# Kernel tuning notes

Measured on AMD Instinct MI355X. Metric: run time of the kernel, lower is better.

The kernel has to match this reference:

```python
import jax, jax.numpy as jnp
import numpy as np

OUT_F = 4096
IN_F = 4096
NNZ_PER_ROW = 205            # ortho_ratio 0.05 * IN_F
NNZ = OUT_F * NNZ_PER_ROW    # 839680
ALPHA = 1.0                  # self.alpha (privacy on)


def setup_inputs() -> dict:
    key = jax.random.key(0)
    k1, k2, k3, k4 = jax.random.split(key, 4)
    x = jax.random.normal(k1, (4, 2048, IN_F), dtype=jnp.float32)
    # offset-uint8 quantized weight (stored here as int32 in [0,256))
    base_packed = jax.random.randint(k2, (OUT_F, IN_F), 0, 256, dtype=jnp.int32)
    # per-output-row dequant scales (robust_max/127 -> small positive values)
    scales = jax.random.uniform(k3, (OUT_F,), dtype=jnp.float32, minval=1e-4, maxval=4e-3)
    # CSR sparse residual: uniform row occupancy, sorted col indices per row
    ortho_vals = (jax.random.normal(k4, (NNZ,), dtype=jnp.float32) * 0.01).astype(jnp.float16)
    rng = np.random.default_rng(0)
    cols = np.sort(rng.integers(0, IN_F, size=(OUT_F, NNZ_PER_ROW)), axis=1)
    ortho_indices = jnp.asarray(cols.reshape(-1).astype(np.int32))
    ortho_ptr = jnp.asarray((np.arange(OUT_F + 1) * NNZ_PER_ROW).astype(np.int32))
    return {
        "x": x,
        "base_packed": base_packed,
        "scales": scales,
        "ortho_vals": ortho_vals,
        "ortho_indices": ortho_indices,
        "ortho_ptr": ortho_ptr,
    }


def reference(x, base_packed, scales, ortho_vals, ortho_indices, ortho_ptr):
    orig_shape = x.shape
    x_flat = x.reshape(-1, IN_F).astype(jnp.float32)          # [T, IN_F]
    # dequantize int8 base weight: (u8 - 128) * scale_row
    w_base = (base_packed.astype(jnp.float32) - 128.0) * scales[:, None]  # [OUT_F, IN_F]
    # expand CSR row pointers -> per-nnz row ids (fixed total length, jit-safe)
    counts = jnp.diff(ortho_ptr)
    rows = jnp.repeat(jnp.arange(OUT_F, dtype=jnp.int32), counts,
                      total_repeat_length=ortho_vals.shape[0])
    # scatter sparse residual into dense weight (matches torch CSR->dense fallback)
    w_ortho = jnp.zeros((OUT_F, IN_F), jnp.float32).at[rows, ortho_indices].add(
        ortho_vals.astype(jnp.float32))
    w = w_base + ALPHA * w_ortho
    out = x_flat @ w.T                                         # [T, OUT_F]
    return out.reshape(orig_shape[:-1] + (OUT_F,)).astype(x.dtype)
```

## Files before the change

### kernel.cpp

```cpp
#include <hip/hip_runtime.h>
#include <hip/hip_fp16.h>

#define IN_F 4096
#define OUT_F 4096
#define TOK 8192
#define NNZ_PER_ROW 205
#define NNZ (OUT_F * NNZ_PER_ROW)

typedef __attribute__((ext_vector_type(8))) _Float16 f16x8;
typedef __attribute__((ext_vector_type(4))) float floatx4;


__global__ __launch_bounds__(256) void cvt_x_kernel(const float* __restrict__ x,
                                                    _Float16* __restrict__ xh) {
    int t = blockIdx.x * 256 + threadIdx.x;
    const float4* p = (const float4*)x + (size_t)t * 2;
    float4 a = p[0], b = p[1];
    f16x8 h;
    h[0] = (_Float16)a.x; h[1] = (_Float16)a.y; h[2] = (_Float16)a.z; h[3] = (_Float16)a.w;
    h[4] = (_Float16)b.x; h[5] = (_Float16)b.y; h[6] = (_Float16)b.z; h[7] = (_Float16)b.w;
    ((f16x8*)xh)[t] = h;
}

__global__ __launch_bounds__(256) void dequant_w_kernel(const int* __restrict__ bp,
                                                        const float* __restrict__ scales,
                                                        _Float16* __restrict__ wh) {
    int t = blockIdx.x * 256 + threadIdx.x;
    int row = t >> 9;
    float s = scales[row];
    const int4* p = (const int4*)bp + (size_t)t * 2;
    int4 a = p[0], b = p[1];
    f16x8 h;
    h[0] = (_Float16)((float)(a.x - 128) * s);
    h[1] = (_Float16)((float)(a.y - 128) * s);
    h[2] = (_Float16)((float)(a.z - 128) * s);
    h[3] = (_Float16)((float)(a.w - 128) * s);
    h[4] = (_Float16)((float)(b.x - 128) * s);
    h[5] = (_Float16)((float)(b.y - 128) * s);
    h[6] = (_Float16)((float)(b.z - 128) * s);
    h[7] = (_Float16)((float)(b.w - 128) * s);
    ((f16x8*)wh)[t] = h;
}

__global__ __launch_bounds__(256) void sparse_add_kernel(const void* __restrict__ vals_raw,
                                                         const int* __restrict__ cols,
                                                         _Float16* __restrict__ wh) {
    int k = blockIdx.x * 256 + threadIdx.x;
    if (k >= NNZ) return;

    const float*    vf = (const float*)vals_raw;
    const _Float16* vh = (const _Float16*)vals_raw;
    float mx = 0.f;
    for (int i = 0; i < 64; ++i) {
        float a = __builtin_fabsf(vf[i]);
        mx = a > mx ? a : mx;
    }
    const bool is_f32 = (mx > 1e-6f) && (mx < 1.0f);

    int row  = k / NNZ_PER_ROW;
    int rbeg = row * NNZ_PER_ROW;
    int rend = rbeg + NNZ_PER_ROW;
    int c    = cols[k];
    if (k != rbeg && cols[k - 1] == c) return;

    float s = is_f32 ? vf[k] : (float)vh[k];
    for (int k2 = k + 1; k2 < rend && cols[k2] == c; ++k2)
        s += is_f32 ? vf[k2] : (float)vh[k2];

    _Float16* p = wh + (size_t)row * IN_F + c;
    *p = (_Float16)((float)*p + s);
}


__global__ __launch_bounds__(256) void gemm_fast_kernel(const _Float16* __restrict__ X,
                                                        const _Float16* __restrict__ W,
                                                        float* __restrict__ out) {
    __shared__ __align__(1024) char smem[32768];
    const int tid  = threadIdx.x;
    const int lane = tid & 63;
    const int w    = tid >> 6;
    const int wm   = w >> 1;
    const int wn   = w & 1;
    const int bm   = blockIdx.y;
    const int bn   = blockIdx.x;

    const int l8 = lane >> 3;
    const int ls = lane & 7;
    const int e  = ls ^ l8;

    floatx4 acc[4][4] = {};

    for (int k0 = 0; k0 < IN_F; k0 += 64) {
#pragma unroll
        for (int j = 0; j < 4; ++j) {
            int c   = w * 4 + j;
            int row = c * 8 + l8;
            const _Float16* gp = X + ((size_t)(bm * 128 + row)) * IN_F + k0 + e * 8;
            char* lp = smem + c * 1024;
            __builtin_amdgcn_global_load_lds((const __attribute__((address_space(1))) void*)gp,
                                             (__attribute__((address_space(3))) void*)lp,
                                             16, 0, 0);
        }
#pragma unroll
        for (int j = 0; j < 4; ++j) {
            int c   = w * 4 + j;
            int row = c * 8 + l8;
            const _Float16* gp = W + ((size_t)(bn * 128 + row)) * IN_F + k0 + e * 8;
            char* lp = smem + 16384 + c * 1024;
            __builtin_amdgcn_global_load_lds((const __attribute__((address_space(1))) void*)gp,
                                             (__attribute__((address_space(3))) void*)lp,
                                             16, 0, 0);
        }
        __syncthreads();

        const int q   = lane >> 4;
        const int r15 = lane & 15;
#pragma unroll
        for (int kk = 0; kk < 64; kk += 32) {
            int j = (kk >> 3) + q;
            f16x8 a[4], b[4];
#pragma unroll
            for (int mt = 0; mt < 4; ++mt) {
                int row = wm * 64 + mt * 16 + r15;
                a[mt] = *(const f16x8*)(smem + row * 128 + ((j ^ (row & 7)) * 16));
            }
#pragma unroll
            for (int nt = 0; nt < 4; ++nt) {
                int row = wn * 64 + nt * 16 + r15;
                b[nt] = *(const f16x8*)(smem + 16384 + row * 128 + ((j ^ (row & 7)) * 16));
            }
#pragma unroll
            for (int mt = 0; mt < 4; ++mt)
#pragma unroll
                for (int nt = 0; nt < 4; ++nt)
                    acc[mt][nt] = __builtin_amdgcn_mfma_f32_16x16x32_f16(a[mt], b[nt],
                                                                         acc[mt][nt], 0, 0, 0);
        }
        __syncthreads();
    }

    const int q   = lane >> 4;
    const int r15 = lane & 15;
#pragma unroll
    for (int mt = 0; mt < 4; ++mt)
#pragma unroll
        for (int nt = 0; nt < 4; ++nt) {
            int o     = bn * 128 + wn * 64 + nt * 16 + r15;
            int tbase = bm * 128 + wm * 64 + mt * 16 + q * 4;
#pragma unroll
            for (int r = 0; r < 4; ++r)
                out[(size_t)(tbase + r) * OUT_F + o] = acc[mt][nt][r];
        }
}


__global__ __launch_bounds__(256) void gemm_kernel(const float* __restrict__ X,
                                                   const _Float16* __restrict__ W,
                                                   float* __restrict__ out) {
    __shared__ __align__(16) _Float16 As[128 * 72];
    __shared__ __align__(16) _Float16 Bs[128 * 72];
    const int tid  = threadIdx.x;
    const int lane = tid & 63;
    const int w    = tid >> 6;
    const int wm   = w >> 1;
    const int wn   = w & 1;
    const int bm   = blockIdx.y;
    const int bn   = blockIdx.x;
    const int srow = tid >> 3;
    const int sch  = tid & 7;

    const float*    Xb = X + (size_t)(bm * 128) * IN_F;
    const _Float16* Wb = W + (size_t)(bn * 128) * IN_F;

    floatx4 acc[4][4] = {};

    for (int k0 = 0; k0 < IN_F; k0 += 64) {
#pragma unroll
        for (int p = 0; p < 4; ++p) {
            int row = p * 32 + srow;
            const float* gp = Xb + (size_t)row * IN_F + k0 + sch * 8;
            float4 u = ((const float4*)gp)[0];
            float4 v = ((const float4*)gp)[1];
            f16x8 h;
            h[0] = (_Float16)u.x; h[1] = (_Float16)u.y;
            h[2] = (_Float16)u.z; h[3] = (_Float16)u.w;
            h[4] = (_Float16)v.x; h[5] = (_Float16)v.y;
            h[6] = (_Float16)v.z; h[7] = (_Float16)v.w;
            *(f16x8*)&As[row * 72 + sch * 8] = h;
        }
#pragma unroll
        for (int p = 0; p < 4; ++p) {
            int row = p * 32 + srow;
            *(f16x8*)&Bs[row * 72 + sch * 8] =
                *(const f16x8*)(Wb + (size_t)row * IN_F + k0 + sch * 8);
        }
        __syncthreads();

        const int q   = lane >> 4;
        const int r15 = lane & 15;
#pragma unroll
        for (int kk = 0; kk < 64; kk += 32) {
            int j = (kk >> 3) + q;
            f16x8 a[4], b[4];
#pragma unroll
            for (int mt = 0; mt < 4; ++mt) {
                int row = wm * 64 + mt * 16 + r15;
                a[mt] = *(const f16x8*)&As[row * 72 + j * 8];
            }
#pragma unroll
            for (int nt = 0; nt < 4; ++nt) {
                int row = wn * 64 + nt * 16 + r15;
                b[nt] = *(const f16x8*)&Bs[row * 72 + j * 8];
            }
#pragma unroll
            for (int mt = 0; mt < 4; ++mt)
#pragma unroll
                for (int nt = 0; nt < 4; ++nt)
                    acc[mt][nt] = __builtin_amdgcn_mfma_f32_16x16x32_f16(a[mt], b[nt],
                                                                         acc[mt][nt], 0, 0, 0);
        }
        __syncthreads();
    }

    const int q   = lane >> 4;
    const int r15 = lane & 15;
#pragma unroll
    for (int mt = 0; mt < 4; ++mt)
#pragma unroll
        for (int nt = 0; nt < 4; ++nt) {
            int o     = bn * 128 + wn * 64 + nt * 16 + r15;
            int tbase = bm * 128 + wm * 64 + mt * 16 + q * 4;
#pragma unroll
            for (int r = 0; r < 4; ++r)
                out[(size_t)(tbase + r) * OUT_F + o] = acc[mt][nt][r];
        }
}


extern "C" void kernel_launch(void* const* d_in, const int* in_sizes, int n_in,
                              void* d_out, int out_size, void* d_ws, size_t ws_size,
                              hipStream_t stream) {
    const float* x      = (const float*)d_in[0];
    const int*   bp     = (const int*)d_in[1];
    const float* scales = (const float*)d_in[2];
    const void*  vals   = (const void*)d_in[3];
    const int*   cols   = (const int*)d_in[4];
    float*       out    = (float*)d_out;

    _Float16* wh = (_Float16*)d_ws;
    const size_t wh_bytes = (size_t)OUT_F * IN_F * 2;
    const size_t xh_bytes = (size_t)TOK * IN_F * 2;

    dequant_w_kernel<<<OUT_F * IN_F / 8 / 256, 256, 0, stream>>>(bp, scales, wh);
    sparse_add_kernel<<<(NNZ + 255) / 256, 256, 0, stream>>>(vals, cols, wh);

    dim3 grid(OUT_F / 128, TOK / 128);
    if (ws_size >= wh_bytes + xh_bytes) {
        _Float16* xh = (_Float16*)((char*)d_ws + wh_bytes);
        cvt_x_kernel<<<TOK * IN_F / 8 / 256, 256, 0, stream>>>(x, xh);
        gemm_fast_kernel<<<grid, 256, 0, stream>>>(xh, wh, out);
    } else {
        gemm_kernel<<<grid, 256, 0, stream>>>(x, wh, out);
    }
}
```

Before: 604.8 us.

## Add 256x256-tile GEMM with async global-to-LDS loads and multi-stage pipelining

Adds a 512-thread GEMM kernel that computes 256x256 output tiles, loads data directly from global memory into LDS through global_load_lds, and uses double-buffered, XOR-swizzled shared memory with 128KB of dynamic LDS. It also remaps block IDs so neighbouring blocks share panels in cache, and raises MFMA priority with s_setprio. The larger tiles are meant to cut global-memory traffic and overlap loads with MFMA work, which should raise matrix-core utilization over the 128x128 kernel. In exchange it needs heavy register and LDS use and hand-written waitcnt/barrier scheduling, and it falls back to the old kernel if the dynamic-LDS attribute cannot be set.

```diff
diff --git a/kernel.cpp b/kernel.cpp
--- a/kernel.cpp
+++ b/kernel.cpp
@@ -72,6 +72,141 @@
 }
 
 
+__global__ __launch_bounds__(512, 2) void gemm256_kernel(const _Float16* __restrict__ X,
+                                                         const _Float16* __restrict__ W,
+                                                         float* __restrict__ out) {
+    extern __shared__ char smem[];
+    const int tid  = threadIdx.x;
+    const int lane = tid & 63;
+    const int w    = tid >> 6;
+    const int wm   = w >> 2;
+    const int wn   = w & 3;
+
+    const int bid = blockIdx.x;
+    const int swz = (bid & 7) * 64 + (bid >> 3);
+    const int bm  = swz >> 4;
+    const int bn  = swz & 15;
+
+    const _Float16* Ap = X + (size_t)(bm * 256) * IN_F;
+    const _Float16* Bp = W + (size_t)(bn * 256) * IN_F;
+
+    int srow[2], sg[2];
+#pragma unroll
+    for (int j = 0; j < 2; ++j) {
+        int ch  = w * 2 + j;
+        int r   = ch * 16 + (lane >> 2);
+        srow[j] = r;
+        sg[j]   = (lane & 3) ^ ((r & 3) ^ ((r >> 2) & 3));
+    }
+
+    auto stage = [&](const _Float16* panel, int ldsOff, int kcol) {
+#pragma unroll
+        for (int j = 0; j < 2; ++j) {
+            const _Float16* gp = panel + (size_t)srow[j] * IN_F + kcol + sg[j] * 8;
+            char* lp = smem + ldsOff + (w * 2 + j) * 1024;
+            __builtin_amdgcn_global_load_lds(
+                (const __attribute__((address_space(1))) void*)gp,
+                (__attribute__((address_space(3))) void*)lp, 16, 0, 0);
+        }
+    };
+
+    const int q    = lane >> 4;
+    const int r15  = lane & 15;
+    const int slot = (q ^ ((r15 & 3) ^ ((r15 >> 2) & 3))) * 16;
+
+    floatx4 acc[8][4] = {};
+    f16x8 afrag[4], bfrag[4];
+
+#define LOAD_B(KKH) do {                                                        \
+    const char* Bb = smem + buf + 32768 + (KKH) * 16384;                        \
+    _Pragma("unroll")                                                           \
+    for (int nt = 0; nt < 4; ++nt)                                              \
+        bfrag[nt] = *(const f16x8*)(Bb + (wn * 64 + nt * 16 + r15) * 64 + slot);\
+} while (0)
+
+#define LOAD_A(MQ, KKH) do {                                                    \
+    const char* Ab = smem + buf + (KKH) * 16384;                                \
+    _Pragma("unroll")                                                           \
+    for (int mt = 0; mt < 4; ++mt)                                              \
+        afrag[mt] = *(const f16x8*)(Ab + (wm * 128 + (MQ) * 64 + mt * 16 + r15) * 64 + slot);\
+} while (0)
+
+#define MFMA_BLK(MQ) do {                                                       \
+    __builtin_amdgcn_s_setprio(1);                                              \
+    _Pragma("unroll")                                                           \
+    for (int mt = 0; mt < 4; ++mt)                                              \
+        _Pragma("unroll")                                                       \
+        for (int nt = 0; nt < 4; ++nt)                                          \
+            acc[(MQ) * 4 + mt][nt] = __builtin_amdgcn_mfma_f32_16x16x32_f16(    \
+                afrag[mt], bfrag[nt], acc[(MQ) * 4 + mt][nt], 0, 0, 0);         \
+    __builtin_amdgcn_s_setprio(0);                                              \
+} while (0)
+
+    stage(Bp, 32768, 0);
+    stage(Ap, 0, 0);
+    stage(Bp, 49152, 32);
+    stage(Ap, 16384, 32);
+    stage(Bp, 65536 + 32768, 64);
+    stage(Ap, 65536 + 0, 64);
+    stage(Bp, 65536 + 49152, 96);
+    asm volatile("s_waitcnt vmcnt(6)" ::: "memory");
+    __builtin_amdgcn_s_barrier();
+
+    for (int kt = 0; kt < 64; ++kt) {
+        const int buf = (kt & 1) << 16;
+        const int ks1 = kt + 1, ks2 = kt + 2;
+        const int b1  = (ks1 & 1) << 16;
+        const int b2  = (ks2 & 1) << 16;
+
+        LOAD_B(0);
+        LOAD_A(0, 0);
+        if (ks1 < 64) stage(Ap, b1 + 16384, ks1 * 64 + 32);
+        __builtin_amdgcn_s_barrier();
+        MFMA_BLK(0);
+        __builtin_amdgcn_s_barrier();
+
+        LOAD_A(1, 0);
+        if (ks2 < 64) stage(Bp, b2 + 32768, ks2 * 64);
+        __builtin_amdgcn_s_barrier();
+        MFMA_BLK(1);
+        __builtin_amdgcn_s_barrier();
+
+        LOAD_B(1);
+        LOAD_A(0, 1);
+        if (ks2 < 64) stage(Ap, b2, ks2 * 64);
+        __builtin_amdgcn_s_barrier();
+        MFMA_BLK(0);
+        __builtin_amdgcn_s_barrier();
+
+        LOAD_A(1, 1);
+        if (ks2 < 64) stage(Bp, b2 + 49152, ks2 * 64 + 32);
+        __builtin_amdgcn_s_barrier();
+        MFMA_BLK(1);
+        if (kt < 62)       asm volatile("s_waitcnt vmcnt(6)" ::: "memory");
+        else if (kt == 62) asm volatile("s_waitcnt vmcnt(0)" ::: "memory");
+        __builtin_amdgcn_s_barrier();
+    }
+
+#undef LOAD_B
+#undef LOAD_A
+#undef MFMA_BLK
+
+#pragma unroll
+    for (int mq = 0; mq < 2; ++mq)
+#pragma unroll
+        for (int mt = 0; mt < 4; ++mt)
+#pragma unroll
+            for (int nt = 0; nt < 4; ++nt) {
+                const int o    = bn * 256 + wn * 64 + nt * 16 + r15;
+                const int trow = bm * 256 + wm * 128 + mq * 64 + mt * 16 + q * 4;
+                const floatx4 v = acc[mq * 4 + mt][nt];
+#pragma unroll
+                for (int r = 0; r < 4; ++r)
+                    out[(size_t)(trow + r) * OUT_F + o] = v[r];
+            }
+}
+
+
 __global__ __launch_bounds__(256) void gemm_fast_kernel(const _Float16* __restrict__ X,
                                                         const _Float16* __restrict__ W,
                                                         float* __restrict__ out) {
@@ -152,7 +287,6 @@
                 out[(size_t)(tbase + r) * OUT_F + o] = acc[mt][nt][r];
         }
 }
-
 
 __global__ __launch_bounds__(256) void gemm_kernel(const float* __restrict__ X,
                                                    const _Float16* __restrict__ W,
@@ -251,15 +385,28 @@
     const size_t wh_bytes = (size_t)OUT_F * IN_F * 2;
     const size_t xh_bytes = (size_t)TOK * IN_F * 2;
 
+    static int use256 = -1;
+    if (use256 < 0) {
+        hipError_t e = hipFuncSetAttribute((const void*)gemm256_kernel,
+                                           hipFuncAttributeMaxDynamicSharedMemorySize,
+                                           131072);
+        use256 = (e == hipSuccess) ? 1 : 0;
+    }
+
     dequant_w_kernel<<<OUT_F * IN_F / 8 / 256, 256, 0, stream>>>(bp, scales, wh);
     sparse_add_kernel<<<(NNZ + 255) / 256, 256, 0, stream>>>(vals, cols, wh);
 
-    dim3 grid(OUT_F / 128, TOK / 128);
     if (ws_size >= wh_bytes + xh_bytes) {
         _Float16* xh = (_Float16*)((char*)d_ws + wh_bytes);
         cvt_x_kernel<<<TOK * IN_F / 8 / 256, 256, 0, stream>>>(x, xh);
-        gemm_fast_kernel<<<grid, 256, 0, stream>>>(xh, wh, out);
+        if (use256) {
+            gemm256_kernel<<<dim3(512), 512, 131072, stream>>>(xh, wh, out);
+        } else {
+            dim3 grid(OUT_F / 128, TOK / 128);
+            gemm_fast_kernel<<<grid, 256, 0, stream>>>(xh, wh, out);
+        }
     } else {
+        dim3 grid(OUT_F / 128, TOK / 128);
         gemm_kernel<<<grid, 256, 0, stream>>>(x, wh, out);
     }
 }
```

Result: faster. 539.6 us (-10.8%).
